# Kernel tuning notes

Hardware: AMD Instinct MI355X
Metric: run time of the kernel (lower is better)

The kernel has to match this reference:

```python
import jax, jax.numpy as jnp
import numpy as np

BLOCK = 64   # init block_size
RATIO = 0.5  # init ratio
GRAY = 128.0


def _make_mask(depth_map, H, W, key):
    """Vectorized equivalent of the per-block python loop.

    Blocks with initial_mask > ratio are kept (all ones). Dropped blocks are
    filled with a random binary region containing round(depth*b*b) zeros,
    chosen uniformly without replacement (torch.randperm semantics ==
    rank-of-uniform-noise < num_zeros).
    """
    nH, nW = H // BLOCK, W // BLOCK
    k1, k2 = jax.random.split(key)
    initial_mask = jax.random.uniform(k1, (nH, nW))           # [nH,nW]
    keep = initial_mask > RATIO                                # blocks kept fully

    d = jnp.where(depth_map.max() > 1.0, depth_map / 255.0, depth_map)
    gray_depth = d.mean(axis=0)                                # [H,W]
    # avg_pool2d with kernel=stride=BLOCK
    avg_depth = gray_depth.reshape(nH, BLOCK, nW, BLOCK).mean(axis=(1, 3))  # [nH,nW]
    num_zeros = jnp.round(avg_depth * (BLOCK * BLOCK)).astype(jnp.int32)    # per block

    # random permutation rank per pixel within each block
    noise = jax.random.uniform(k2, (nH, nW, BLOCK * BLOCK))
    ranks = jnp.argsort(jnp.argsort(noise, axis=-1), axis=-1)               # [nH,nW,b*b]
    region = (ranks >= num_zeros[..., None]).astype(jnp.float32)            # zeros at low ranks

    blocks = jnp.where(keep[..., None], 1.0, region)           # [nH,nW,b*b]
    mask = blocks.reshape(nH, nW, BLOCK, BLOCK).transpose(0, 2, 1, 3).reshape(H, W)
    return mask


def setup_inputs() -> dict:
    key = jax.random.key(0)
    k1, k2 = jax.random.split(key)
    img = jax.random.uniform(k1, (3, 2048, 4096), dtype=jnp.float32) * 255.0
    depth_map = jax.random.uniform(k2, (3, 2048, 4096), dtype=jnp.float32)
    return {"img": img, "depth_map": depth_map}


def reference(img, depth_map):
    C, H, W = img.shape
    mask = _make_mask(depth_map, H, W, jax.random.key(42))     # [H,W]
    # resize to (H,W) is a no-op since mask is already full resolution
    return img * mask + GRAY * (1.0 - mask)
```

## Files before the change

kernel.cpp:

```cpp
#include <hip/hip_runtime.h>
#include <stdint.h>

static constexpr int kH  = 2048;
static constexpr int kW  = 4096;
static constexpr int kHW = kH * kW;
static constexpr int kNH = kH / 64;
static constexpr int kNW = kW / 64;
static constexpr int kNB = kNH * kNW;
static constexpr int kBB = 64 * 64;
static constexpr int kGrayN = kNB * kBB;
static constexpr float kGray = 128.0f;

__host__ __device__ inline void tf2x32(uint32_t k0, uint32_t k1,
                                       uint32_t x0, uint32_t x1,
                                       uint32_t& o0, uint32_t& o1) {
  uint32_t ks2 = 0x1BD11BDAu ^ k0 ^ k1;
  x0 += k0; x1 += k1;
#define ROTL(v, d) (((v) << (d)) | ((v) >> (32 - (d))))
#define RND(R) { x0 += x1; x1 = ROTL(x1, R); x1 ^= x0; }
  RND(13) RND(15) RND(26) RND(6)
  x0 += k1;  x1 += ks2 + 1u;
  RND(17) RND(29) RND(16) RND(24)
  x0 += ks2; x1 += k0 + 2u;
  RND(13) RND(15) RND(26) RND(6)
  x0 += k0;  x1 += k1 + 3u;
  RND(17) RND(29) RND(16) RND(24)
  x0 += k1;  x1 += ks2 + 4u;
  RND(13) RND(15) RND(26) RND(6)
  x0 += ks2; x1 += k0 + 5u;
  o0 = x0; o1 = x1;
#undef RND
#undef ROTL
}

__device__ inline uint32_t rbits(uint32_t ka, uint32_t kb, uint32_t idx) {
  uint32_t o0, o1;
  tf2x32(ka, kb, 0u, idx, o0, o1);
  return o0 ^ o1;
}

__device__ inline bool keep_block(uint32_t k1a, uint32_t k1b, int b) {
  uint32_t v = rbits(k1a, k1b, (uint32_t)b) >> 9;
  return v > 0x400000u;
}

__global__ __launch_bounds__(256) void k1_depth(const float* __restrict__ depth,
                                                float* __restrict__ Gu,
                                                float* __restrict__ Gs,
                                                float* __restrict__ Bmax,
                                                uint32_t k1a, uint32_t k1b_) {
  __shared__ float red[256];
  const int b = blockIdx.x, t = threadIdx.x;
  const int bi = b >> 6, bj = b & 63;
  const int y0 = bi * 64, x0 = bj * 64;
  const bool keep = keep_block(k1a, k1b_, b);
  const float4* d4 = reinterpret_cast<const float4*>(depth);

  float mx = 0.0f;
  #pragma unroll
  for (int it = 0; it < 4; ++it) {
    int idx = it * 256 + t;
    int r = idx >> 4, cq = idx & 15;
    uint32_t a4 = (uint32_t)(y0 + r) * (kW / 4) + (uint32_t)(x0 / 4 + cq);
    float4 d0 = d4[a4];
    float4 d1 = d4[a4 + kHW / 4];
    float4 d2 = d4[a4 + 2 * (kHW / 4)];
    mx = fmaxf(mx, fmaxf(fmaxf(fmaxf(d0.x, d0.y), fmaxf(d0.z, d0.w)),
               fmaxf(fmaxf(fmaxf(d1.x, d1.y), fmaxf(d1.z, d1.w)),
                     fmaxf(fmaxf(d2.x, d2.y), fmaxf(d2.z, d2.w)))));
    if (!keep) {
      uint32_t p4 = (uint32_t)b * (kBB / 4) + (uint32_t)idx;
      float4 u, s;
      u.x = ((d0.x + d1.x) + d2.x) / 3.0f;
      u.y = ((d0.y + d1.y) + d2.y) / 3.0f;
      u.z = ((d0.z + d1.z) + d2.z) / 3.0f;
      u.w = ((d0.w + d1.w) + d2.w) / 3.0f;
      s.x = ((d0.x / 255.0f + d1.x / 255.0f) + d2.x / 255.0f) / 3.0f;
      s.y = ((d0.y / 255.0f + d1.y / 255.0f) + d2.y / 255.0f) / 3.0f;
      s.z = ((d0.z / 255.0f + d1.z / 255.0f) + d2.z / 255.0f) / 3.0f;
      s.w = ((d0.w / 255.0f + d1.w / 255.0f) + d2.w / 255.0f) / 3.0f;
      reinterpret_cast<float4*>(Gu)[p4] = u;
      reinterpret_cast<float4*>(Gs)[p4] = s;
    }
  }
  red[t] = mx;
  __syncthreads();
  for (int s = 128; s > 0; s >>= 1) {
    if (t < s) red[t] = fmaxf(red[t], red[t + s]);
    __syncthreads();
  }
  if (t == 0) Bmax[b] = red[0];
}

__global__ __launch_bounds__(64) void kchain(const float* __restrict__ G,
                                             const float* __restrict__ Bmax,
                                             float* __restrict__ S,
                                             uint32_t k1a, uint32_t k1b_) {
  const int w = blockIdx.x, lane = threadIdx.x;

  float m = 0.0f;
  #pragma unroll
  for (int i = 0; i < kNB / 64; ++i) m = fmaxf(m, Bmax[lane + i * 64]);
  #pragma unroll
  for (int d = 32; d >= 1; d >>= 1) m = fmaxf(m, __shfl_xor(m, d, 64));
  const bool flag = m > 1.0f;

  uint32_t bits = 0;
  int c = 0;
  #pragma unroll
  for (int j = 0; j < 32; ++j) {
    int b = lane * 32 + j;
    if (!keep_block(k1a, k1b_, b)) { bits |= (1u << j); ++c; }
  }
  int P = c;
  #pragma unroll
  for (int d = 1; d < 64; d <<= 1) {
    int v = __shfl_up(P, d, 64);
    if (lane >= d) P += v;
  }
  const int total = __shfl(P, 63, 64);
  P -= c;

  const int r0 = 2 * w, r1 = 2 * w + 1;
  int b0c = -1, b1c = -1;
  if (r0 >= P && r0 < P + c) {
    uint32_t bb = bits;
    for (int i = r0 - P; i > 0; --i) bb &= bb - 1;
    b0c = lane * 32 + __ffs(bb) - 1;
  }
  if (r1 >= P && r1 < P + c) {
    uint32_t bb = bits;
    for (int i = r1 - P; i > 0; --i) bb &= bb - 1;
    b1c = lane * 32 + __ffs(bb) - 1;
  }
  unsigned long long m0 = __ballot(b0c >= 0);
  unsigned long long m1 = __ballot(b1c >= 0);
  const int blk0 = (r0 < total && m0) ? __shfl(b0c, (int)(__ffsll(m0) - 1), 64) : -1;
  const int blk1 = (r1 < total && m1) ? __shfl(b1c, (int)(__ffsll(m1) - 1), 64) : -1;

  const int blk = (lane == 0) ? blk0 : blk1;
  if (lane < 2 && blk >= 0) {
    const float4* g4 = reinterpret_cast<const float4*>(G) +
                       (flag ? (uint32_t)(kGrayN / 4) : 0u) + (uint32_t)blk * (kBB / 4);

    float4 buf[32];
    #pragma unroll
    for (int i = 0; i < 32; ++i) buf[i] = g4[i];
    uint32_t gp = 32;

    float acc = 0.0f;
    for (int outer = 0; outer < 31; ++outer) {
      #pragma unroll
      for (int i = 0; i < 32; ++i) {
        float4 v = buf[i];
        buf[i] = g4[gp + i];
        acc += v.x; acc += v.y; acc += v.z; acc += v.w;
      }
      gp += 32;
    }
    #pragma unroll
    for (int i = 0; i < 32; ++i) {
      float4 v = buf[i];
      acc += v.x; acc += v.y; acc += v.z; acc += v.w;
    }
    S[blk] = acc;
  }
}

__global__ __launch_bounds__(256) void k3_fused(const float* __restrict__ img,
                                                float* __restrict__ out,
                                                const float* __restrict__ S,
                                                uint32_t k1a, uint32_t k1b_,
                                                uint32_t k2a, uint32_t k2b) {
  __shared__ uint32_t hist[256];
  __shared__ uint32_t cand[64];
  __shared__ uint32_t sh[4];
  const int b = blockIdx.x, t = threadIdx.x;
  const int bi = b >> 6, bj = b & 63;
  const int y0 = bi * 64, x0 = bj * 64;
  const float4* img4 = reinterpret_cast<const float4*>(img);
  float4* out4 = reinterpret_cast<float4*>(out);

  int nz;
  if (keep_block(k1a, k1b_, b)) {
    nz = 0;
  } else {
    float s = S[b];
    nz = (int)rintf(s);
    if (nz < 0) nz = 0;
    if (nz > kBB) nz = kBB;
  }

  const int row0 = t >> 4, cq = t & 15;

  if (nz == 0 || nz == kBB) {
    const bool fill = (nz == kBB);
    const float4 g4v = make_float4(kGray, kGray, kGray, kGray);
    #pragma unroll
    for (int it = 0; it < 4; ++it) {
      uint32_t a4 = (uint32_t)(y0 + it * 16 + row0) * (kW / 4) + (uint32_t)(x0 / 4 + cq);
      #pragma unroll
      for (int ch = 0; ch < 3; ++ch) {
        uint32_t a = a4 + (uint32_t)ch * (kHW / 4);
        out4[a] = fill ? g4v : img4[a];
      }
    }
    return;
  }

  const uint32_t base = (uint32_t)b * (uint32_t)kBB;
  uint32_t v[4][4];
  #pragma unroll
  for (int it = 0; it < 4; ++it) {
    uint32_t p = (uint32_t)((it * 16 + row0) * 64 + cq * 4);
    #pragma unroll
    for (int j = 0; j < 4; ++j) v[it][j] = rbits(k2a, k2b, base + p + j) >> 9;
  }

  hist[t] = 0;
  if (t == 0) sh[3] = 0;
  __syncthreads();
  #pragma unroll
  for (int it = 0; it < 4; ++it)
    #pragma unroll
    for (int j = 0; j < 4; ++j) atomicAdd(&hist[v[it][j] >> 15], 1u);
  __syncthreads();
  {
    uint32_t h = hist[t];
    for (int s = 1; s < 256; s <<= 1) {
      uint32_t add = (t >= s) ? hist[t - s] : 0;
      __syncthreads();
      hist[t] += add;
      __syncthreads();
    }
    uint32_t inc = hist[t], exc = inc - h;
    if (inc >= (uint32_t)nz && exc < (uint32_t)nz) { sh[0] = (uint32_t)t; sh[1] = (uint32_t)nz - exc; }
  }
  __syncthreads();
  const uint32_t B1 = sh[0], rr2 = sh[1];

  hist[t] = 0;
  __syncthreads();
  #pragma unroll
  for (int it = 0; it < 4; ++it)
    #pragma unroll
    for (int j = 0; j < 4; ++j) {
      uint32_t vv = v[it][j];
      if ((vv >> 15) == B1) atomicAdd(&hist[(vv >> 7) & 0xFFu], 1u);
    }
  __syncthreads();
  {
    uint32_t h = hist[t];
    for (int s = 1; s < 256; s <<= 1) {
      uint32_t add = (t >= s) ? hist[t - s] : 0;
      __syncthreads();
      hist[t] += add;
      __syncthreads();
    }
    uint32_t inc = hist[t], exc = inc - h;
    if (inc >= rr2 && exc < rr2) { sh[0] = (uint32_t)t; sh[1] = rr2 - exc; }
  }
  __syncthreads();
  const uint32_t pref16 = (B1 << 8) | sh[0];
  const uint32_t rr3 = sh[1];

  #pragma unroll
  for (int it = 0; it < 4; ++it)
    #pragma unroll
    for (int j = 0; j < 4; ++j) {
      uint32_t vv = v[it][j];
      if ((vv >> 7) == pref16) {
        uint32_t p = (uint32_t)((it * 16 + row0) * 64 + cq * 4 + j);
        uint32_t slot = atomicAdd(&sh[3], 1u);
        if (slot < 64u) cand[slot] = ((vv & 0x7Fu) << 12) | p;
      }
    }
  __syncthreads();
  const uint32_t m = sh[3] < 64u ? sh[3] : 64u;
  if (t < (int)m) {
    uint32_t key = cand[t], rank = 0;
    for (uint32_t q = 0; q < m; ++q) rank += (cand[q] < key) ? 1u : 0u;
    if (rank == rr3 - 1) sh[2] = key;
  }
  __syncthreads();
  const uint32_t T3 = sh[2];

  #pragma unroll
  for (int it = 0; it < 4; ++it) {
    uint32_t p = (uint32_t)((it * 16 + row0) * 64 + cq * 4);
    uint32_t kmask = 0;
    #pragma unroll
    for (int j = 0; j < 4; ++j) {
      uint32_t vv = v[it][j];
      uint32_t pre = vv >> 7;
      bool zero = (pre < pref16) ||
                  (pre == pref16 && ((((vv & 0x7Fu) << 12) | (p + j)) <= T3));
      if (!zero) kmask |= (1u << j);
    }
    uint32_t a4 = (uint32_t)(y0 + it * 16 + row0) * (kW / 4) + (uint32_t)(x0 / 4 + cq);
    #pragma unroll
    for (int ch = 0; ch < 3; ++ch) {
      uint32_t a = a4 + (uint32_t)ch * (kHW / 4);
      float4 vf = img4[a];
      float4 o;
      o.x = (kmask & 1u) ? vf.x : kGray;
      o.y = (kmask & 2u) ? vf.y : kGray;
      o.z = (kmask & 4u) ? vf.z : kGray;
      o.w = (kmask & 8u) ? vf.w : kGray;
      out4[a] = o;
    }
  }
}

extern "C" void kernel_launch(void* const* d_in, const int* in_sizes, int n_in,
                              void* d_out, int out_size, void* d_ws, size_t ws_size,
                              hipStream_t stream) {
  const float* img   = (const float*)d_in[0];
  const float* depth = (const float*)d_in[1];
  float* out = (float*)d_out;

  float* Gu = out;
  float* Gs = out + kGrayN;

  float* S    = (float*)d_ws;
  float* Bmax = S + kNB;

  uint32_t k1a, k1b_, k2a, k2b;
  tf2x32(0u, 42u, 0u, 0u, k1a, k1b_);
  tf2x32(0u, 42u, 0u, 1u, k2a, k2b);

  k1_depth<<<kNB, 256, 0, stream>>>(depth, Gu, Gs, Bmax, k1a, k1b_);
  kchain  <<<kNB / 2, 64, 0, stream>>>(out, Bmax, S, k1a, k1b_);
  k3_fused<<<kNB, 256, 0, stream>>>(img, out, S, k1a, k1b_, k2a, k2b);
}
```

Baseline: 114.1 us.

## Drop gray scratch buffers, recompute gray in chain kernel, copy kept blocks early

Stops writing the two per-pixel gray-depth scratch arrays into the output buffer. The chain kernel now re-reads depth for its two dropped blocks and stages the gray values in LDS. Kept blocks are copied img->out inside the depth kernel, so the final kernel only handles dropped blocks, and its LDS-barrier prefix scans become wave-shuffle scans. This removes scratch write and read traffic plus many barriers, at the cost of a second depth read for dropped blocks and a larger first kernel.

```diff
diff --git a/kernel.cpp b/kernel.cpp
--- a/kernel.cpp
+++ b/kernel.cpp
@@ -8,7 +8,6 @@
 static constexpr int kNW = kW / 64;
 static constexpr int kNB = kNH * kNW;
 static constexpr int kBB = 64 * 64;
-static constexpr int kGrayN = kNB * kBB;
 static constexpr float kGray = 128.0f;
 
 __host__ __device__ inline void tf2x32(uint32_t k0, uint32_t k1,
@@ -45,8 +44,8 @@
 }
 
 __global__ __launch_bounds__(256) void k1_depth(const float* __restrict__ depth,
-                                                float* __restrict__ Gu,
-                                                float* __restrict__ Gs,
+                                                const float* __restrict__ img,
+                                                float* __restrict__ out,
                                                 float* __restrict__ Bmax,
                                                 uint32_t k1a, uint32_t k1b_) {
   __shared__ float red[256];
@@ -54,7 +53,9 @@
   const int bi = b >> 6, bj = b & 63;
   const int y0 = bi * 64, x0 = bj * 64;
   const bool keep = keep_block(k1a, k1b_, b);
-  const float4* d4 = reinterpret_cast<const float4*>(depth);
+  const float4* d4   = reinterpret_cast<const float4*>(depth);
+  const float4* img4 = reinterpret_cast<const float4*>(img);
+  float4* out4 = reinterpret_cast<float4*>(out);
 
   float mx = 0.0f;
   #pragma unroll
@@ -68,20 +69,6 @@
     mx = fmaxf(mx, fmaxf(fmaxf(fmaxf(d0.x, d0.y), fmaxf(d0.z, d0.w)),
                fmaxf(fmaxf(fmaxf(d1.x, d1.y), fmaxf(d1.z, d1.w)),
                      fmaxf(fmaxf(d2.x, d2.y), fmaxf(d2.z, d2.w)))));
-    if (!keep) {
-      uint32_t p4 = (uint32_t)b * (kBB / 4) + (uint32_t)idx;
-      float4 u, s;
-      u.x = ((d0.x + d1.x) + d2.x) / 3.0f;
-      u.y = ((d0.y + d1.y) + d2.y) / 3.0f;
-      u.z = ((d0.z + d1.z) + d2.z) / 3.0f;
-      u.w = ((d0.w + d1.w) + d2.w) / 3.0f;
-      s.x = ((d0.x / 255.0f + d1.x / 255.0f) + d2.x / 255.0f) / 3.0f;
-      s.y = ((d0.y / 255.0f + d1.y / 255.0f) + d2.y / 255.0f) / 3.0f;
-      s.z = ((d0.z / 255.0f + d1.z / 255.0f) + d2.z / 255.0f) / 3.0f;
-      s.w = ((d0.w / 255.0f + d1.w / 255.0f) + d2.w / 255.0f) / 3.0f;
-      reinterpret_cast<float4*>(Gu)[p4] = u;
-      reinterpret_cast<float4*>(Gs)[p4] = s;
-    }
   }
   red[t] = mx;
   __syncthreads();
@@ -90,13 +77,27 @@
     __syncthreads();
   }
   if (t == 0) Bmax[b] = red[0];
-}
-
-__global__ __launch_bounds__(64) void kchain(const float* __restrict__ G,
+
+  if (keep) {
+    #pragma unroll
+    for (int i = 0; i < 12; ++i) {
+      int f = i * 256 + t;
+      int ch = f >> 10, idx = f & 1023;
+      int r = idx >> 4, cq = idx & 15;
+      uint32_t a = (uint32_t)(y0 + r) * (kW / 4) + (uint32_t)(x0 / 4 + cq)
+                 + (uint32_t)ch * (kHW / 4);
+      out4[a] = img4[a];
+    }
+  }
+}
+
+__global__ __launch_bounds__(64) void kchain(const float* __restrict__ depth,
                                              const float* __restrict__ Bmax,
                                              float* __restrict__ S,
                                              uint32_t k1a, uint32_t k1b_) {
+  __shared__ float4 gl4[2048];
   const int w = blockIdx.x, lane = threadIdx.x;
+  const float4* d4 = reinterpret_cast<const float4*>(depth);
 
   float m = 0.0f;
   #pragma unroll
@@ -105,8 +106,7 @@
   for (int d = 32; d >= 1; d >>= 1) m = fmaxf(m, __shfl_xor(m, d, 64));
   const bool flag = m > 1.0f;
 
-  uint32_t bits = 0;
-  int c = 0;
+  uint32_t bits = 0; int c = 0;
   #pragma unroll
   for (int j = 0; j < 32; ++j) {
     int b = lane * 32 + j;
@@ -120,7 +120,6 @@
   }
   const int total = __shfl(P, 63, 64);
   P -= c;
-
   const int r0 = 2 * w, r1 = 2 * w + 1;
   int b0c = -1, b1c = -1;
   if (r0 >= P && r0 < P + c) {
@@ -137,73 +136,103 @@
   unsigned long long m1 = __ballot(b1c >= 0);
   const int blk0 = (r0 < total && m0) ? __shfl(b0c, (int)(__ffsll(m0) - 1), 64) : -1;
   const int blk1 = (r1 < total && m1) ? __shfl(b1c, (int)(__ffsll(m1) - 1), 64) : -1;
-
-  const int blk = (lane == 0) ? blk0 : blk1;
-  if (lane < 2 && blk >= 0) {
-    const float4* g4 = reinterpret_cast<const float4*>(G) +
-                       (flag ? (uint32_t)(kGrayN / 4) : 0u) + (uint32_t)blk * (kBB / 4);
-
-    float4 buf[32];
-    #pragma unroll
-    for (int i = 0; i < 32; ++i) buf[i] = g4[i];
-    uint32_t gp = 32;
-
+  if (blk0 < 0) return;
+
+  #pragma unroll
+  for (int cidx = 0; cidx < 2; ++cidx) {
+    const int blk = (cidx == 0) ? blk0 : blk1;
+    if (blk < 0) break;
+    const int bbi = blk >> 6, bbj = blk & 63;
+    const float4* dbase = d4 + (uint32_t)(bbi * 64) * (kW / 4) + (uint32_t)(bbj * 16);
+    #pragma unroll
+    for (int k = 0; k < 16; ++k) {
+      int s = k * 64 + lane;
+      int r = s >> 4, cq = s & 15;
+      uint32_t a4 = (uint32_t)r * (kW / 4) + (uint32_t)cq;
+      float4 d0 = dbase[a4];
+      float4 d1 = dbase[a4 + kHW / 4];
+      float4 d2 = dbase[a4 + 2 * (kHW / 4)];
+      float4 g;
+      if (flag) {
+        g.x = ((d0.x / 255.0f + d1.x / 255.0f) + d2.x / 255.0f) / 3.0f;
+        g.y = ((d0.y / 255.0f + d1.y / 255.0f) + d2.y / 255.0f) / 3.0f;
+        g.z = ((d0.z / 255.0f + d1.z / 255.0f) + d2.z / 255.0f) / 3.0f;
+        g.w = ((d0.w / 255.0f + d1.w / 255.0f) + d2.w / 255.0f) / 3.0f;
+      } else {
+        g.x = ((d0.x + d1.x) + d2.x) / 3.0f;
+        g.y = ((d0.y + d1.y) + d2.y) / 3.0f;
+        g.z = ((d0.z + d1.z) + d2.z) / 3.0f;
+        g.w = ((d0.w + d1.w) + d2.w) / 3.0f;
+      }
+      gl4[cidx * 1024 + s] = g;
+    }
+  }
+  __syncthreads();
+
+  if (lane < 2) {
+    const int blk = (lane == 0) ? blk0 : blk1;
+    const float4* g4 = gl4 + lane * 1024;
+    float4 buf[16];
+    #pragma unroll
+    for (int i = 0; i < 16; ++i) buf[i] = g4[i];
+    int gp = 16;
     float acc = 0.0f;
-    for (int outer = 0; outer < 31; ++outer) {
+    for (int outer = 0; outer < 63; ++outer) {
       #pragma unroll
-      for (int i = 0; i < 32; ++i) {
+      for (int i = 0; i < 16; ++i) {
         float4 v = buf[i];
         buf[i] = g4[gp + i];
         acc += v.x; acc += v.y; acc += v.z; acc += v.w;
       }
-      gp += 32;
-    }
-    #pragma unroll
-    for (int i = 0; i < 32; ++i) {
+      gp += 16;
+    }
+    #pragma unroll
+    for (int i = 0; i < 16; ++i) {
       float4 v = buf[i];
       acc += v.x; acc += v.y; acc += v.z; acc += v.w;
     }
-    S[blk] = acc;
-  }
-}
-
-__global__ __launch_bounds__(256) void k3_fused(const float* __restrict__ img,
-                                                float* __restrict__ out,
-                                                const float* __restrict__ S,
-                                                uint32_t k1a, uint32_t k1b_,
-                                                uint32_t k2a, uint32_t k2b) {
+    if (blk >= 0) S[blk] = acc;
+  }
+}
+
+__global__ __launch_bounds__(256) void k3_drop(const float* __restrict__ img,
+                                               float* __restrict__ out,
+                                               const float* __restrict__ S,
+                                               uint32_t k1a, uint32_t k1b_,
+                                               uint32_t k2a, uint32_t k2b) {
   __shared__ uint32_t hist[256];
   __shared__ uint32_t cand[64];
   __shared__ uint32_t sh[4];
+  __shared__ uint32_t wtot[4];
   const int b = blockIdx.x, t = threadIdx.x;
+  const int lane = t & 63, wv = t >> 6;
+  if (keep_block(k1a, k1b_, b)) return;
+
   const int bi = b >> 6, bj = b & 63;
   const int y0 = bi * 64, x0 = bj * 64;
   const float4* img4 = reinterpret_cast<const float4*>(img);
   float4* out4 = reinterpret_cast<float4*>(out);
 
   int nz;
-  if (keep_block(k1a, k1b_, b)) {
-    nz = 0;
-  } else {
-    float s = S[b];
-    nz = (int)rintf(s);
+  {
+    float sv = S[b];
+    nz = (int)rintf(sv);
     if (nz < 0) nz = 0;
     if (nz > kBB) nz = kBB;
   }
-
   const int row0 = t >> 4, cq = t & 15;
 
   if (nz == 0 || nz == kBB) {
     const bool fill = (nz == kBB);
     const float4 g4v = make_float4(kGray, kGray, kGray, kGray);
     #pragma unroll
-    for (int it = 0; it < 4; ++it) {
-      uint32_t a4 = (uint32_t)(y0 + it * 16 + row0) * (kW / 4) + (uint32_t)(x0 / 4 + cq);
-      #pragma unroll
-      for (int ch = 0; ch < 3; ++ch) {
-        uint32_t a = a4 + (uint32_t)ch * (kHW / 4);
-        out4[a] = fill ? g4v : img4[a];
-      }
+    for (int i = 0; i < 12; ++i) {
+      int f = i * 256 + t;
+      int ch = f >> 10, idx = f & 1023;
+      int r = idx >> 4, cc = idx & 15;
+      uint32_t a = (uint32_t)(y0 + r) * (kW / 4) + (uint32_t)(x0 / 4 + cc)
+                 + (uint32_t)ch * (kHW / 4);
+      out4[a] = fill ? g4v : img4[a];
     }
     return;
   }
@@ -226,21 +255,23 @@
     for (int j = 0; j < 4; ++j) atomicAdd(&hist[v[it][j] >> 15], 1u);
   __syncthreads();
   {
-    uint32_t h = hist[t];
-    for (int s = 1; s < 256; s <<= 1) {
-      uint32_t add = (t >= s) ? hist[t - s] : 0;
-      __syncthreads();
-      hist[t] += add;
-      __syncthreads();
-    }
-    uint32_t inc = hist[t], exc = inc - h;
+    uint32_t h = hist[t], sc = h;
+    #pragma unroll
+    for (int d = 1; d < 64; d <<= 1) {
+      uint32_t vv = __shfl_up(sc, d, 64);
+      if (lane >= d) sc += vv;
+    }
+    if (lane == 63) wtot[wv] = sc;
+    __syncthreads();
+    uint32_t pre = 0;
+    for (int k = 0; k < wv; ++k) pre += wtot[k];
+    uint32_t inc = sc + pre, exc = inc - h;
     if (inc >= (uint32_t)nz && exc < (uint32_t)nz) { sh[0] = (uint32_t)t; sh[1] = (uint32_t)nz - exc; }
-  }
-  __syncthreads();
+    hist[t] = 0;
+    __syncthreads();
+  }
   const uint32_t B1 = sh[0], rr2 = sh[1];
 
-  hist[t] = 0;
-  __syncthreads();
   #pragma unroll
   for (int it = 0; it < 4; ++it)
     #pragma unroll
@@ -250,17 +281,20 @@
     }
   __syncthreads();
   {
-    uint32_t h = hist[t];
-    for (int s = 1; s < 256; s <<= 1) {
-      uint32_t add = (t >= s) ? hist[t - s] : 0;
-      __syncthreads();
-      hist[t] += add;
-      __syncthreads();
-    }
-    uint32_t inc = hist[t], exc = inc - h;
+    uint32_t h = hist[t], sc = h;
+    #pragma unroll
+    for (int d = 1; d < 64; d <<= 1) {
+      uint32_t vv = __shfl_up(sc, d, 64);
+      if (lane >= d) sc += vv;
+    }
+    if (lane == 63) wtot[wv] = sc;
+    __syncthreads();
+    uint32_t pre = 0;
+    for (int k = 0; k < wv; ++k) pre += wtot[k];
+    uint32_t inc = sc + pre, exc = inc - h;
     if (inc >= rr2 && exc < rr2) { sh[0] = (uint32_t)t; sh[1] = rr2 - exc; }
-  }
-  __syncthreads();
+    __syncthreads();
+  }
   const uint32_t pref16 = (B1 << 8) | sh[0];
   const uint32_t rr3 = sh[1];
 
@@ -319,9 +353,6 @@
   const float* depth = (const float*)d_in[1];
   float* out = (float*)d_out;
 
-  float* Gu = out;
-  float* Gs = out + kGrayN;
-
   float* S    = (float*)d_ws;
   float* Bmax = S + kNB;
 
@@ -329,7 +360,7 @@
   tf2x32(0u, 42u, 0u, 0u, k1a, k1b_);
   tf2x32(0u, 42u, 0u, 1u, k2a, k2b);
 
-  k1_depth<<<kNB, 256, 0, stream>>>(depth, Gu, Gs, Bmax, k1a, k1b_);
-  kchain  <<<kNB / 2, 64, 0, stream>>>(out, Bmax, S, k1a, k1b_);
-  k3_fused<<<kNB, 256, 0, stream>>>(img, out, S, k1a, k1b_, k2a, k2b);
-}
+  k1_depth<<<kNB, 256, 0, stream>>>(depth, img, out, Bmax, k1a, k1b_);
+  kchain  <<<kNB / 2, 64, 0, stream>>>(depth, Bmax, S, k1a, k1b_);
+  k3_drop <<<kNB, 256, 0, stream>>>(img, out, S, k1a, k1b_, k2a, k2b);
+}
```

Result: slower. 130.3 us (+14.2%).
